# Performance work log

Hardware: AMD Instinct MI355X
Metric: run time of the kernel (lower is better)

The kernel has to match this reference:

```python
import jax, jax.numpy as jnp
import numpy as np

ALPHA = 0.2  # LeakyReLU negative slope
NEG_INF = -9e15

def setup_inputs() -> dict:
    key = jax.random.key(0)
    k1, k2, k3, k4 = jax.random.split(key, 4)
    N, IN_F, OUT_F = 12288, 256, 128
    h = jax.random.normal(k1, (N, IN_F), dtype=jnp.float32)
    adj = jax.random.randint(k2, (N, N), 0, 2, dtype=jnp.int32)
    # Xavier-uniform-like init with gain 1.414
    limW = 1.414 * np.sqrt(6.0 / (IN_F + OUT_F))
    W = jax.random.uniform(k3, (IN_F, OUT_F), dtype=jnp.float32, minval=-limW, maxval=limW)
    lima = 1.414 * np.sqrt(6.0 / (2 * OUT_F + 1))
    a = jax.random.uniform(k4, (2 * OUT_F, 1), dtype=jnp.float32, minval=-lima, maxval=lima)
    return {"h": h, "adj": adj, "W": W, "a": a}

def reference(h, adj, W, a):
    out_f = W.shape[1]
    Wh = h @ W                      # [N, out_f]
    Wh1 = Wh @ a[:out_f, :]         # [N, 1]
    Wh2 = Wh @ a[out_f:, :]         # [N, 1]
    e = Wh1 + Wh2.T                 # [N, N] broadcast-add scores
    e = jnp.where(e > 0, e, ALPHA * e)  # LeakyReLU
    scores = jnp.where(adj > 0, e, NEG_INF)
    attention = jax.nn.softmax(scores, axis=1)  # dropout is identity at inference
    h_prime = attention @ Wh        # [N, out_f]
    return jax.nn.elu(h_prime)      # concat=True -> ELU
```

## Files before the change

### kernel.cpp

```cpp
#include <hip/hip_runtime.h>

#define NN   12288
#define FIN  256
#define FOUT 128
#define ALPHA 0.2f

typedef __attribute__((ext_vector_type(8))) _Float16 half8v;
typedef __attribute__((ext_vector_type(4))) float float4v;
typedef __attribute__((ext_vector_type(4))) int   int4v;


__global__ __launch_bounds__(128) void k_wh(
    const float* __restrict__ h,
    const float* __restrict__ W,
    const float* __restrict__ a,
    _Float16* __restrict__ WhT2,
    float* __restrict__ Wh1, float* __restrict__ Wh2,
    float* __restrict__ mxArr)
{
    __shared__ float sP1[2][16], sP2[2][16];
    const int t = threadIdx.x;
    const int row0 = blockIdx.x * 16;

    float acc[16];
    #pragma unroll
    for (int r = 0; r < 16; ++r) acc[r] = 0.f;

    const float* hb = h + (size_t)row0 * FIN;
    for (int k = 0; k < FIN; k += 4) {
        const float w0 = W[(k + 0) * FOUT + t];
        const float w1 = W[(k + 1) * FOUT + t];
        const float w2 = W[(k + 2) * FOUT + t];
        const float w3 = W[(k + 3) * FOUT + t];
        #pragma unroll
        for (int r = 0; r < 16; ++r) {
            const float4v hv = *(const float4v*)(hb + r * FIN + k);
            float s = acc[r];
            s = fmaf(hv.x, w0, s);
            s = fmaf(hv.y, w1, s);
            s = fmaf(hv.z, w2, s);
            s = fmaf(hv.w, w3, s);
            acc[r] = s;
        }
    }

    half8v pk0, pk1;
    #pragma unroll
    for (int r = 0; r < 8; ++r)  pk0[r] = (_Float16)acc[r];
    #pragma unroll
    for (int r = 0; r < 8; ++r)  pk1[r] = (_Float16)acc[8 + r];
    _Float16* dst = WhT2 + (size_t)(row0 >> 5) * 4096 + t * 32 + (row0 & 16);
    *(half8v*)(dst)     = pk0;
    *(half8v*)(dst + 8) = pk1;

    const float a1t = a[t];
    const float a2t = a[FOUT + t];
    const int lane = t & 63, wv = t >> 6;
    #pragma unroll
    for (int r = 0; r < 16; ++r) {
        float v1 = acc[r] * a1t;
        float v2 = acc[r] * a2t;
        #pragma unroll
        for (int off = 1; off < 64; off <<= 1) {
            v1 += __shfl_xor(v1, off, 64);
            v2 += __shfl_xor(v2, off, 64);
        }
        if (lane == 0) { sP1[wv][r] = v1; sP2[wv][r] = v2; }
    }
    __syncthreads();
    if (t < 16) {
        const float v1 = sP1[0][t] + sP1[1][t];
        float v2 = sP2[0][t] + sP2[1][t];
        Wh1[row0 + t] = v1;
        Wh2[row0 + t] = v2;
        #pragma unroll
        for (int off = 1; off < 16; off <<= 1)
            v2 = fmaxf(v2, __shfl_xor(v2, off, 64));
        if (t == 0) mxArr[blockIdx.x] = v2;
    }
}

static __device__ __forceinline__ half8v build_p(
    const int4v a0, const int4v a1, const float* wvv,
    const float wh1, const float M, float& S)
{
    const int av[8] = {a0.x, a0.y, a0.z, a0.w, a1.x, a1.y, a1.z, a1.w};
    half8v af;
    #pragma unroll
    for (int jj = 0; jj < 8; ++jj) {
        float e = wh1 + wvv[jj];
        e = fmaxf(e, ALPHA * e);
        const float p = av[jj] ? __expf(e - M) : 0.f;
        af[jj] = (_Float16)p;
        S += p;
    }
    return af;
}

static __device__ __forceinline__ float wave_gmax(
    const float* __restrict__ mxArr, int nmx, int lane)
{
    float mv = -1e30f;
    for (int idx = lane; idx < nmx; idx += 64) mv = fmaxf(mv, mxArr[idx]);
    #pragma unroll
    for (int off = 1; off < 64; off <<= 1)
        mv = fmaxf(mv, __shfl_xor(mv, off, 64));
    return mv;
}

__global__ __launch_bounds__(64, 2) void k_attn(
    const int* __restrict__ adj,
    const _Float16* __restrict__ WhT2,
    const float* __restrict__ Wh1, const float* __restrict__ Wh2,
    const float* __restrict__ mxArr, int nmx,
    float* __restrict__ pC, float* __restrict__ pS)
{
    const int lane = threadIdx.x;
    const int m    = lane & 15;
    const int q    = lane >> 4;
    const int rowbase = blockIdx.x * 32;
    const int J    = gridDim.y;
    const int jy   = blockIdx.y;
    const int jlen = NN / J;
    const int jbeg = jy * jlen;

    const float mxv = wave_gmax(mxArr, nmx, lane);

    float wh1[2], Mi[2];
    const int* rowp[2];
    #pragma unroll
    for (int rg = 0; rg < 2; ++rg) {
        const int row = rowbase + rg * 16 + m;
        wh1[rg] = Wh1[row];
        const float tm = wh1[rg] + mxv;
        Mi[rg] = fmaxf(tm, ALPHA * tm);
        rowp[rg] = adj + (size_t)row * NN;
    }

    float4v c[2][8];
    #pragma unroll
    for (int rg = 0; rg < 2; ++rg)
        #pragma unroll
        for (int t = 0; t < 8; ++t) c[rg][t] = (float4v){0.f, 0.f, 0.f, 0.f};
    float S[2] = {0.f, 0.f};

    int4v na0[2], na1[2];
    float4v nw0, nw1;
    {
        const int jb = jbeg + q * 8;
        #pragma unroll
        for (int rg = 0; rg < 2; ++rg) {
            na0[rg] = __builtin_nontemporal_load((const int4v*)(rowp[rg] + jb));
            na1[rg] = __builtin_nontemporal_load((const int4v*)(rowp[rg] + jb + 4));
        }
        nw0 = *(const float4v*)(Wh2 + jb);
        nw1 = *(const float4v*)(Wh2 + jb + 4);
    }

    const int iters = jlen / 32;
    for (int it = 0; it < iters; ++it) {
        const int j0 = jbeg + it * 32;

        const int4v a0[2] = {na0[0], na0[1]};
        const int4v a1[2] = {na1[0], na1[1]};
        const float4v w0 = nw0, w1 = nw1;

        if (it + 1 < iters) {
            const int jb = j0 + 32 + q * 8;
            #pragma unroll
            for (int rg = 0; rg < 2; ++rg) {
                na0[rg] = __builtin_nontemporal_load((const int4v*)(rowp[rg] + jb));
                na1[rg] = __builtin_nontemporal_load((const int4v*)(rowp[rg] + jb + 4));
            }
            nw0 = *(const float4v*)(Wh2 + jb);
            nw1 = *(const float4v*)(Wh2 + jb + 4);
        }

        const _Float16* tp = WhT2 + (size_t)(j0 >> 5) * 4096;
        half8v b[8];
        #pragma unroll
        for (int t = 0; t < 8; ++t)
            b[t] = *(const half8v*)(tp + (t * 16 + m) * 32 + q * 8);

        const float wvv[8] = {w0.x, w0.y, w0.z, w0.w, w1.x, w1.y, w1.z, w1.w};

        #pragma unroll
        for (int rg = 0; rg < 2; ++rg) {
            const half8v af = build_p(a0[rg], a1[rg], wvv, wh1[rg], Mi[rg], S[rg]);
            #pragma unroll
            for (int t = 0; t < 8; ++t)
                c[rg][t] = __builtin_amdgcn_mfma_f32_16x16x32_f16(af, b[t], c[rg][t], 0, 0, 0);
        }
    }

    #pragma unroll
    for (int rg = 0; rg < 2; ++rg) {
        S[rg] += __shfl_xor(S[rg], 16, 64);
        S[rg] += __shfl_xor(S[rg], 32, 64);
        if (q == 0) pS[(size_t)jy * NN + rowbase + rg * 16 + m] = S[rg];
    }

    #pragma unroll
    for (int rg = 0; rg < 2; ++rg)
        #pragma unroll
        for (int t = 0; t < 8; ++t)
            #pragma unroll
            for (int reg = 0; reg < 4; ++reg) {
                const int row = rowbase + rg * 16 + q * 4 + reg;
                pC[((size_t)jy * NN + row) * FOUT + t * 16 + m] = c[rg][t][reg];
            }
}

__global__ __launch_bounds__(256) void k_reduce(
    const float* __restrict__ pC, const float* __restrict__ pS,
    float* __restrict__ out, int J)
{
    const int idx = blockIdx.x * 256 + threadIdx.x;
    const int row = idx >> 5;
    const int c4  = (idx & 31) * 4;
    float4v acc = (float4v){0.f, 0.f, 0.f, 0.f};
    float S = 0.f;
    for (int j = 0; j < J; ++j) {
        const float4v v = *(const float4v*)(pC + ((size_t)j * NN + row) * FOUT + c4);
        acc.x += v.x; acc.y += v.y; acc.z += v.z; acc.w += v.w;
        S += pS[(size_t)j * NN + row];
    }
    const float inv = 1.f / fmaxf(S, 1e-30f);
    float4v r;
    #pragma unroll
    for (int k = 0; k < 4; ++k) {
        const float v = acc[k] * inv;
        r[k] = (v > 0.f) ? v : (__expf(v) - 1.f);
    }
    *(float4v*)(out + (size_t)row * FOUT + c4) = r;
}

__global__ __launch_bounds__(64, 2) void k_attn_fb(
    const int* __restrict__ adj,
    const _Float16* __restrict__ WhT2,
    const float* __restrict__ Wh1, const float* __restrict__ Wh2,
    const float* __restrict__ mxArr, int nmx,
    float* __restrict__ out)
{
    const int lane = threadIdx.x;
    const int m    = lane & 15;
    const int q    = lane >> 4;
    const int rowbase = blockIdx.x * 32;

    const float mxv = wave_gmax(mxArr, nmx, lane);

    float wh1[2], Mi[2];
    const int* rowp[2];
    #pragma unroll
    for (int rg = 0; rg < 2; ++rg) {
        const int row = rowbase + rg * 16 + m;
        wh1[rg] = Wh1[row];
        const float tm = wh1[rg] + mxv;
        Mi[rg] = fmaxf(tm, ALPHA * tm);
        rowp[rg] = adj + (size_t)row * NN;
    }

    float4v c[2][8];
    #pragma unroll
    for (int rg = 0; rg < 2; ++rg)
        #pragma unroll
        for (int t = 0; t < 8; ++t) c[rg][t] = (float4v){0.f, 0.f, 0.f, 0.f};
    float S[2] = {0.f, 0.f};

    for (int j0 = 0; j0 < NN; j0 += 32) {
        const int jb = j0 + q * 8;
        int4v a0[2], a1[2];
        #pragma unroll
        for (int rg = 0; rg < 2; ++rg) {
            a0[rg] = __builtin_nontemporal_load((const int4v*)(rowp[rg] + jb));
            a1[rg] = __builtin_nontemporal_load((const int4v*)(rowp[rg] + jb + 4));
        }
        const _Float16* tp = WhT2 + (size_t)(j0 >> 5) * 4096;
        half8v b[8];
        #pragma unroll
        for (int t = 0; t < 8; ++t)
            b[t] = *(const half8v*)(tp + (t * 16 + m) * 32 + q * 8);
        const float4v w0 = *(const float4v*)(Wh2 + jb);
        const float4v w1 = *(const float4v*)(Wh2 + jb + 4);
        const float wvv[8] = {w0.x, w0.y, w0.z, w0.w, w1.x, w1.y, w1.z, w1.w};
        #pragma unroll
        for (int rg = 0; rg < 2; ++rg) {
            const half8v af = build_p(a0[rg], a1[rg], wvv, wh1[rg], Mi[rg], S[rg]);
            #pragma unroll
            for (int t = 0; t < 8; ++t)
                c[rg][t] = __builtin_amdgcn_mfma_f32_16x16x32_f16(af, b[t], c[rg][t], 0, 0, 0);
        }
    }

    #pragma unroll
    for (int rg = 0; rg < 2; ++rg) {
        S[rg] += __shfl_xor(S[rg], 16, 64);
        S[rg] += __shfl_xor(S[rg], 32, 64);
        #pragma unroll
        for (int reg = 0; reg < 4; ++reg) {
            const int mloc = q * 4 + reg;
            const float Sr = __shfl(S[rg], mloc, 64);
            const float inv = 1.f / fmaxf(Sr, 1e-30f);
            #pragma unroll
            for (int t = 0; t < 8; ++t) {
                const float v = c[rg][t][reg] * inv;
                out[(size_t)(rowbase + rg * 16 + mloc) * FOUT + t * 16 + m] =
                    (v > 0.f) ? v : (__expf(v) - 1.f);
            }
        }
    }
}

extern "C" void kernel_launch(void* const* d_in, const int* in_sizes, int n_in,
                              void* d_out, int out_size, void* d_ws, size_t ws_size,
                              hipStream_t stream) {
    const float* h   = (const float*)d_in[0];
    const int*   adj = (const int*)d_in[1];
    const float* W   = (const float*)d_in[2];
    const float* a   = (const float*)d_in[3];
    float* out = (float*)d_out;

    char* ws = (char*)d_ws;
    float* Wh1   = (float*)ws;
    float* Wh2   = (float*)(ws + 49152);
    float* mxArr = (float*)(ws + 98304);
    _Float16* WhT2 = (_Float16*)(ws + 101376);
    const size_t base_need = 101376ULL + 3145728ULL;
    const int NB = NN / 16;

    int J = 8;
    while (J > 1 &&
           base_need + (size_t)J * NN * 4 + (size_t)J * NN * FOUT * 4 > ws_size)
        J >>= 1;
    const bool ok =
        base_need + (size_t)NN * 4 + (size_t)NN * FOUT * 4 <= ws_size;

    k_wh<<<NB, 128, 0, stream>>>(h, W, a, WhT2, Wh1, Wh2, mxArr);
    if (ok) {
        float* pS = (float*)(ws + base_need);
        float* pC = pS + (size_t)J * NN;
        k_attn<<<dim3(NN / 32, J), 64, 0, stream>>>(adj, WhT2, Wh1, Wh2,
                                                    mxArr, NB, pC, pS);
        k_reduce<<<(NN * (FOUT / 4)) / 256, 256, 0, stream>>>(pC, pS, out, J);
    } else {
        k_attn_fb<<<NN / 32, 64, 0, stream>>>(adj, WhT2, Wh1, Wh2, mxArr, NB, out);
    }
}
```

Baseline: 930.7 us.

## Pack adjacency into bitmask in a pre-pass before attention kernel

Adds a kernel that reads the int32 adjacency matrix once with coalesced wide loads and packs it into one bit per entry. The attention kernel then reads 32-bit mask words instead of strided int4 loads of adj. This is meant to replace the attention kernel's scattered per-row reads with fully coalesced streaming. The cost is an extra launch plus a full read of adj and a small mask write, so total adj traffic stays about the same.

```diff
diff --git a/kernel.cpp b/kernel.cpp
--- a/kernel.cpp
+++ b/kernel.cpp
@@ -4,6 +4,7 @@
 #define FIN  256
 #define FOUT 128
 #define ALPHA 0.2f
+#define NWORDS (NN / 32)
 
 typedef __attribute__((ext_vector_type(8))) _Float16 half8v;
 typedef __attribute__((ext_vector_type(4))) float float4v;
@@ -80,6 +81,46 @@
     }
 }
 
+__global__ __launch_bounds__(256) void k_pack(
+    const int* __restrict__ adj, unsigned int* __restrict__ maskR)
+{
+    const int wid  = blockIdx.x * 4 + (threadIdx.x >> 6);
+    const int lane = threadIdx.x & 63;
+    const int row  = wid / 6;
+    const int ck   = wid - row * 6;
+    const int4v* src =
+        (const int4v*)(adj + (size_t)row * NN + ck * 2048 + lane * 32);
+    int4v v[8];
+    #pragma unroll
+    for (int u = 0; u < 8; ++u)
+        v[u] = __builtin_nontemporal_load(src + u);
+    unsigned int w = 0;
+    #pragma unroll
+    for (int u = 0; u < 8; ++u) {
+        w |= (v[u].x != 0 ? 1u : 0u) << (u * 4 + 0);
+        w |= (v[u].y != 0 ? 1u : 0u) << (u * 4 + 1);
+        w |= (v[u].z != 0 ? 1u : 0u) << (u * 4 + 2);
+        w |= (v[u].w != 0 ? 1u : 0u) << (u * 4 + 3);
+    }
+    maskR[(size_t)row * NWORDS + ck * 64 + lane] = w;
+}
+
+static __device__ __forceinline__ half8v build_p_bits(
+    unsigned int bits, const float* wvv,
+    const float wh1, const float M, float& S)
+{
+    half8v af;
+    #pragma unroll
+    for (int jj = 0; jj < 8; ++jj) {
+        float e = wh1 + wvv[jj];
+        e = fmaxf(e, ALPHA * e);
+        const float p = ((bits >> jj) & 1u) ? __expf(e - M) : 0.f;
+        af[jj] = (_Float16)p;
+        S += p;
+    }
+    return af;
+}
+
 static __device__ __forceinline__ half8v build_p(
     const int4v a0, const int4v a1, const float* wvv,
     const float wh1, const float M, float& S)
@@ -109,7 +150,7 @@
 }
 
 __global__ __launch_bounds__(64, 2) void k_attn(
-    const int* __restrict__ adj,
+    const unsigned int* __restrict__ maskR,
     const _Float16* __restrict__ WhT2,
     const float* __restrict__ Wh1, const float* __restrict__ Wh2,
     const float* __restrict__ mxArr, int nmx,
@@ -127,14 +168,14 @@
     const float mxv = wave_gmax(mxArr, nmx, lane);
 
     float wh1[2], Mi[2];
-    const int* rowp[2];
+    const unsigned int* mrow[2];
     #pragma unroll
     for (int rg = 0; rg < 2; ++rg) {
         const int row = rowbase + rg * 16 + m;
         wh1[rg] = Wh1[row];
         const float tm = wh1[rg] + mxv;
         Mi[rg] = fmaxf(tm, ALPHA * tm);
-        rowp[rg] = adj + (size_t)row * NN;
+        mrow[rg] = maskR + (size_t)row * NWORDS;
     }
 
     float4v c[2][8];
@@ -144,36 +185,28 @@
         for (int t = 0; t < 8; ++t) c[rg][t] = (float4v){0.f, 0.f, 0.f, 0.f};
     float S[2] = {0.f, 0.f};
 
-    int4v na0[2], na1[2];
+    unsigned int nmw0, nmw1;
     float4v nw0, nw1;
     {
-        const int jb = jbeg + q * 8;
-        #pragma unroll
-        for (int rg = 0; rg < 2; ++rg) {
-            na0[rg] = __builtin_nontemporal_load((const int4v*)(rowp[rg] + jb));
-            na1[rg] = __builtin_nontemporal_load((const int4v*)(rowp[rg] + jb + 4));
-        }
-        nw0 = *(const float4v*)(Wh2 + jb);
-        nw1 = *(const float4v*)(Wh2 + jb + 4);
+        nmw0 = mrow[0][jbeg >> 5];
+        nmw1 = mrow[1][jbeg >> 5];
+        nw0 = *(const float4v*)(Wh2 + jbeg + q * 8);
+        nw1 = *(const float4v*)(Wh2 + jbeg + q * 8 + 4);
     }
 
     const int iters = jlen / 32;
     for (int it = 0; it < iters; ++it) {
         const int j0 = jbeg + it * 32;
 
-        const int4v a0[2] = {na0[0], na0[1]};
-        const int4v a1[2] = {na1[0], na1[1]};
+        const unsigned int mw0 = nmw0, mw1 = nmw1;
         const float4v w0 = nw0, w1 = nw1;
 
         if (it + 1 < iters) {
-            const int jb = j0 + 32 + q * 8;
-            #pragma unroll
-            for (int rg = 0; rg < 2; ++rg) {
-                na0[rg] = __builtin_nontemporal_load((const int4v*)(rowp[rg] + jb));
-                na1[rg] = __builtin_nontemporal_load((const int4v*)(rowp[rg] + jb + 4));
-            }
-            nw0 = *(const float4v*)(Wh2 + jb);
-            nw1 = *(const float4v*)(Wh2 + jb + 4);
+            const int jn = j0 + 32;
+            nmw0 = mrow[0][jn >> 5];
+            nmw1 = mrow[1][jn >> 5];
+            nw0 = *(const float4v*)(Wh2 + jn + q * 8);
+            nw1 = *(const float4v*)(Wh2 + jn + q * 8 + 4);
         }
 
         const _Float16* tp = WhT2 + (size_t)(j0 >> 5) * 4096;
@@ -184,13 +217,14 @@
 
         const float wvv[8] = {w0.x, w0.y, w0.z, w0.w, w1.x, w1.y, w1.z, w1.w};
 
-        #pragma unroll
-        for (int rg = 0; rg < 2; ++rg) {
-            const half8v af = build_p(a0[rg], a1[rg], wvv, wh1[rg], Mi[rg], S[rg]);
-            #pragma unroll
-            for (int t = 0; t < 8; ++t)
-                c[rg][t] = __builtin_amdgcn_mfma_f32_16x16x32_f16(af, b[t], c[rg][t], 0, 0, 0);
-        }
+        const half8v af0 = build_p_bits(mw0 >> (q * 8), wvv, wh1[0], Mi[0], S[0]);
+        #pragma unroll
+        for (int t = 0; t < 8; ++t)
+            c[0][t] = __builtin_amdgcn_mfma_f32_16x16x32_f16(af0, b[t], c[0][t], 0, 0, 0);
+        const half8v af1 = build_p_bits(mw1 >> (q * 8), wvv, wh1[1], Mi[1], S[1]);
+        #pragma unroll
+        for (int t = 0; t < 8; ++t)
+            c[1][t] = __builtin_amdgcn_mfma_f32_16x16x32_f16(af1, b[t], c[1][t], 0, 0, 0);
     }
 
     #pragma unroll
@@ -325,7 +359,8 @@
     float* Wh2   = (float*)(ws + 49152);
     float* mxArr = (float*)(ws + 98304);
     _Float16* WhT2 = (_Float16*)(ws + 101376);
-    const size_t base_need = 101376ULL + 3145728ULL;
+    unsigned int* maskR = (unsigned int*)(ws + 3247104);
+    const size_t base_need = 3247104ULL + 18874368ULL;
     const int NB = NN / 16;
 
     int J = 8;
@@ -339,7 +374,8 @@
     if (ok) {
         float* pS = (float*)(ws + base_need);
         float* pC = pS + (size_t)J * NN;
-        k_attn<<<dim3(NN / 32, J), 64, 0, stream>>>(adj, WhT2, Wh1, Wh2,
+        k_pack<<<(NN * 6) / 4, 256, 0, stream>>>(adj, maskR);
+        k_attn<<<dim3(NN / 32, J), 64, 0, stream>>>(maskR, WhT2, Wh1, Wh2,
                                                     mxArr, NB, pC, pS);
         k_reduce<<<(NN * (FOUT / 4)) / 256, 256, 0, stream>>>(pC, pS, out, J);
     } else {
```

Result: slower. 1.091 ms (+17.3%).
